# Kernel optimization log

Hardware: AMD Instinct MI355X
Metric: run time of the kernel (lower is better)

The kernel has to match this reference:

```python
import jax, jax.numpy as jnp
import numpy as np

EPS = 1e-16
LOG_2PI = float(np.log(2.0 * np.pi))
DUMMY = -2.0 * float(np.log(10.0))  # dummy component logit / log-prob


def setup_inputs() -> dict:
    key = jax.random.key(0)
    k1, k2, k3, k4, k5 = jax.random.split(key, 5)
    B, N, V, D = 32, 1024, 512, 4
    x = jax.random.normal(k1, (B, N, D), dtype=jnp.float32)
    votes = jax.random.normal(k2, (B, V, D), dtype=jnp.float32)
    # positive stds in [0.1, 1.0)
    scales = jax.random.uniform(k3, (B, V), dtype=jnp.float32) * 0.9 + 0.1
    vote_presence_prob = jax.random.uniform(k4, (B, V), dtype=jnp.float32)
    presence = jax.random.uniform(k5, (B, N), dtype=jnp.float32)
    return {"x": x, "votes": votes, "scales": scales,
            "vote_presence_prob": vote_presence_prob,
            "presence": presence, "n_votes": 16}


def reference(x, votes, scales, vote_presence_prob, presence, n_votes):
    B, N, D = x.shape
    V = votes.shape[1]
    # Broadcast Normal log-prob: x [B,N,1,D] vs votes [B,1,V,D], scale [B,1,V,1]
    sig = scales[:, None, :, None]
    z = (x[:, :, None, :] - votes[:, None, :, :]) / sig
    lp_per_dim = -0.5 * z * z - jnp.log(sig) - 0.5 * LOG_2PI
    vote_log_prob = jnp.sum(lp_per_dim, axis=-1)                       # [B,N,V]
    vote_log_prob = jnp.concatenate(
        [vote_log_prob, jnp.full((B, N, 1), DUMMY, vote_log_prob.dtype)], axis=2)  # [B,N,V+1]

    mixing_logits = jnp.log(vote_presence_prob + EPS)                  # safe_log, [B,V]
    mixing_logits = jnp.concatenate(
        [mixing_logits, jnp.full((B, 1), DUMMY, mixing_logits.dtype)], axis=1)     # [B,V+1]
    mixing_log_prob = jax.nn.log_softmax(mixing_logits, axis=1)        # [B,V+1]

    posterior = mixing_log_prob[:, None, :] + vote_log_prob            # [B,N,V+1]
    mixture_lp_per_comp = jax.scipy.special.logsumexp(posterior, axis=2)  # [B,N]
    mixture_lp_per_comp = mixture_lp_per_comp * presence
    log_prob = jnp.sum(mixture_lp_per_comp)                            # scalar

    winning_vote_idx = jnp.argmax(posterior[:, :, :-1], axis=2)        # [B,N]
    winner = jnp.take_along_axis(votes, winning_vote_idx[:, :, None], axis=1)  # [B,N,D]
    winner_pres = jnp.take_along_axis(vote_presence_prob, winning_vote_idx, axis=1)  # [B,N]
    vote_presence = (mixing_logits[:, :-1] > mixing_logits[:, -1:]).astype(jnp.float32)  # [B,V]
    is_from_capsule = winning_vote_idx // n_votes                      # [B,N]
    posterior_mixing_probs = jax.nn.softmax(posterior, axis=-1)[..., :-1]  # [B,N,V]

    return (log_prob, vote_presence, winner, winner_pres, is_from_capsule,
            mixing_logits, mixing_log_prob, jnp.zeros_like(winner),
            jnp.zeros_like(winner_pres), posterior_mixing_probs)
```

## Files before the change

kernel.cpp:

```cpp
#include <hip/hip_runtime.h>

typedef float v2f __attribute__((ext_vector_type(2)));

#define FEPS 1e-16f
#define LOG_2PI 1.8378770664093453f
#define DUMMYV -4.605170185988091f
#define LOG2E 1.4426950408889634f
#define LN2 0.6931471805599453f

constexpr int B = 32, N = 1024, V = 512;

constexpr long long OFF_LOGPROB    = 0;
constexpr long long OFF_VOTEPRES   = 1;
constexpr long long OFF_WINNER     = OFF_VOTEPRES + (long long)B * V;
constexpr long long OFF_WINNERPRES = OFF_WINNER + (long long)B * N * 4;
constexpr long long OFF_ISFROM     = OFF_WINNERPRES + (long long)B * N;
constexpr long long OFF_MLOGITS    = OFF_ISFROM + (long long)B * N;
constexpr long long OFF_MLOGPROB   = OFF_MLOGITS + (long long)B * (V + 1);
constexpr long long OFF_ZW         = OFF_MLOGPROB + (long long)B * (V + 1);
constexpr long long OFF_ZWP        = OFF_ZW + (long long)B * N * 4;
constexpr long long OFF_PMP        = OFF_ZWP + (long long)B * N;

__device__ __forceinline__ float fexp2(float x) {
#if __has_builtin(__builtin_amdgcn_exp2f)
    return __builtin_amdgcn_exp2f(x);
#else
    return __expf(x * LN2);
#endif
}
__device__ __forceinline__ float frcp(float x) {
#if __has_builtin(__builtin_amdgcn_rcpf)
    return __builtin_amdgcn_rcpf(x);
#else
    return 1.0f / x;
#endif
}

template<int RN> __device__ __forceinline__ float dppRorF(float x) {
    return __int_as_float(__builtin_amdgcn_update_dpp(
        0, __float_as_int(x), 0x120 | RN, 0xF, 0xF, false));
}
template<int RN> __device__ __forceinline__ int dppRorI(int x) {
    return __builtin_amdgcn_update_dpp(0, x, 0x120 | RN, 0xF, 0xF, false);
}

__device__ __forceinline__ float waveMaxF(float m) {
    m = fmaxf(m, dppRorF<1>(m));
    m = fmaxf(m, dppRorF<2>(m));
    m = fmaxf(m, dppRorF<4>(m));
    m = fmaxf(m, dppRorF<8>(m));
    m = fmaxf(m, __shfl_xor(m, 16));
    m = fmaxf(m, __shfl_xor(m, 32));
    return m;
}
__device__ __forceinline__ float waveSumF(float s) {
    s += dppRorF<1>(s);
    s += dppRorF<2>(s);
    s += dppRorF<4>(s);
    s += dppRorF<8>(s);
    s += __shfl_xor(s, 16);
    s += __shfl_xor(s, 32);
    return s;
}
__device__ __forceinline__ int waveMinI(int v) {
    int o;
    o = dppRorI<1>(v); v = o < v ? o : v;
    o = dppRorI<2>(v); v = o < v ? o : v;
    o = dppRorI<4>(v); v = o < v ? o : v;
    o = dppRorI<8>(v); v = o < v ? o : v;
    o = __shfl_xor(v, 16); v = o < v ? o : v;
    o = __shfl_xor(v, 32); v = o < v ? o : v;
    return v;
}

__global__ __launch_bounds__(256) void k_fused(const float* __restrict__ x,
                                               const float* __restrict__ votes,
                                               const float* __restrict__ scales,
                                               const float* __restrict__ vpp,
                                               const float* __restrict__ presence,
                                               const int* __restrict__ nvp,
                                               float* __restrict__ out,
                                               float* __restrict__ ws) {
    __shared__ float s_part[4];
    const int b = blockIdx.y, t = threadIdx.x, w = t >> 6, lane = t & 63;
    const long long bV = (long long)b * V;
    const float4* votes4 = reinterpret_cast<const float4*>(votes) + bV;

    float lg[8], lsv[8];
    float4 vt[8];
    #pragma unroll
    for (int k = 0; k < 8; ++k) {
        int v = k * 64 + lane;
        vt[k]  = votes4[v];
        lsv[k] = scales[bV + v];
        lg[k]  = __logf(vpp[bV + v] + FEPS);
    }

    float mm = lg[0];
    #pragma unroll
    for (int k = 1; k < 8; ++k) mm = fmaxf(mm, lg[k]);
    float M = fmaxf(waveMaxF(mm), DUMMYV);
    float ss = 0.f;
    #pragma unroll
    for (int k = 0; k < 8; ++k) ss += __expf(lg[k] - M);
    float S = waveSumF(ss) + __expf(DUMMYV - M);
    float lse = M + __logf(S);
    float dummy_post = DUMMYV + (DUMMYV - lse);

    if (blockIdx.x == 0 && w == 0) {
        #pragma unroll
        for (int k = 0; k < 8; ++k) {
            int v = k * 64 + lane;
            out[OFF_MLOGITS  + (long long)b * (V + 1) + v] = lg[k];
            out[OFF_MLOGPROB + (long long)b * (V + 1) + v] = lg[k] - lse;
            out[OFF_VOTEPRES + bV + v] = (lg[k] > DUMMYV) ? 1.0f : 0.0f;
        }
        if (lane == 0) {
            out[OFF_MLOGITS  + (long long)b * (V + 1) + V] = DUMMYV;
            out[OFF_MLOGPROB + (long long)b * (V + 1) + V] = DUMMYV - lse;
        }
    }

    v2f c2[4], hk[4], hvx[4], hvy[4], hvz[4], hvw[4];
    #pragma unroll
    for (int i = 0; i < 4; ++i) {
        float cc[2], kk[2], ax[2], ay[2], az[2], aw[2];
        #pragma unroll
        for (int h = 0; h < 2; ++h) {
            int k = 2 * i + h;
            float sv  = lsv[k];
            float inv = frcp(sv);
            float hh  = 0.5f * inv * inv;
            float c   = lg[k] - 4.0f * __logf(sv) - 2.0f * LOG_2PI - lse;
            float4 vv = vt[k];
            float v2  = vv.x * vv.x + vv.y * vv.y + vv.z * vv.z + vv.w * vv.w;
            cc[h] = (c - hh * v2 - dummy_post) * LOG2E;
            kk[h] = -hh * LOG2E;
            float g = 2.0f * hh * LOG2E;
            ax[h] = g * vv.x; ay[h] = g * vv.y; az[h] = g * vv.z; aw[h] = g * vv.w;
        }
        c2[i].x = cc[0];  c2[i].y = cc[1];
        hk[i].x = kk[0];  hk[i].y = kk[1];
        hvx[i].x = ax[0]; hvx[i].y = ax[1];
        hvy[i].x = ay[0]; hvy[i].y = ay[1];
        hvz[i].x = az[0]; hvz[i].y = az[1];
        hvw[i].x = aw[0]; hvw[i].y = aw[1];
    }

    const float4* x4 = reinterpret_cast<const float4*>(x) + (long long)b * N;
    const long long pmpB = OFF_PMP + ((long long)b * N) * V;
    int nv = nvp[0];
    float acc = 0.f;

    #pragma unroll 2
    for (int iter = 0; iter < 8; ++iter) {
        int n = blockIdx.x * 32 + iter * 4 + w;
        long long bn = (long long)b * N + n;
        float4 xv = x4[n];
        float px2 = xv.x * xv.x + xv.y * xv.y + xv.z * xv.z + xv.w * xv.w;
        v2f P2; P2.x = px2;  P2.y = px2;
        v2f Xx; Xx.x = xv.x; Xx.y = xv.x;
        v2f Xy; Xy.x = xv.y; Xy.y = xv.y;
        v2f Xz; Xz.x = xv.z; Xz.y = xv.z;
        v2f Xw; Xw.x = xv.w; Xw.y = xv.w;

        float p2s[8];
        #pragma unroll
        for (int i = 0; i < 4; ++i) {
            v2f tt = c2[i];
            tt += hk[i]  * P2;
            tt += hvx[i] * Xx;
            tt += hvy[i] * Xy;
            tt += hvz[i] * Xz;
            tt += hvw[i] * Xw;
            p2s[2 * i]     = tt.x;
            p2s[2 * i + 1] = tt.y;
        }

        float t1 = fmaxf(fmaxf(p2s[0], p2s[1]), p2s[2]);
        float t2 = fmaxf(fmaxf(p2s[3], p2s[4]), p2s[5]);
        float t3 = fmaxf(fmaxf(p2s[6], p2s[7]), t1);
        float m_in = fmaxf(t2, t3);
        float Mrow = waveMaxF(m_in);

        int kw = 7;
        #pragma unroll
        for (int k = 6; k >= 0; --k) kw = (p2s[k] == Mrow) ? k : kw;
        int cand = (m_in == Mrow) ? (kw * 64 + lane) : 0x7fffffff;
        int bi = waveMinI(cand);

        float e[8];
        float se = 0.f;
        #pragma unroll
        for (int k = 0; k < 8; ++k) { e[k] = fexp2(p2s[k]); se += e[k]; }
        se = waveSumF(se);
        float total = se + 1.0f;
        float rt = frcp(total);

        long long pb = pmpB + (long long)n * V;
        #pragma unroll
        for (int k = 0; k < 8; ++k)
            out[pb + k * 64 + lane] = e[k] * rt;

        if (lane == 0) {
            acc += (dummy_post + LN2 * __log2f(total)) * presence[bn];
            float4 wv = votes4[bi];
            out[OFF_WINNER + bn * 4 + 0] = wv.x;
            out[OFF_WINNER + bn * 4 + 1] = wv.y;
            out[OFF_WINNER + bn * 4 + 2] = wv.z;
            out[OFF_WINNER + bn * 4 + 3] = wv.w;
            out[OFF_WINNERPRES + bn]     = vpp[bV + bi];
            out[OFF_ISFROM + bn]         = (float)((nv == 16) ? (bi >> 4) : (bi / nv));
        }
        if (lane == 1) {
            out[OFF_ZW + bn * 4 + 0] = 0.f;
            out[OFF_ZW + bn * 4 + 1] = 0.f;
            out[OFF_ZW + bn * 4 + 2] = 0.f;
            out[OFF_ZW + bn * 4 + 3] = 0.f;
            out[OFF_ZWP + bn]        = 0.f;
        }
    }

    if (lane == 0) s_part[w] = acc;
    __syncthreads();
    if (t == 0)
        ws[(long long)b * gridDim.x + blockIdx.x] =
            s_part[0] + s_part[1] + s_part[2] + s_part[3];
}

__global__ __launch_bounds__(256) void k_reduce(const float* __restrict__ ws,
                                                float* __restrict__ out, int count) {
    __shared__ float sred[256];
    int t = threadIdx.x;
    float s = 0.f;
    for (int i = t; i < count; i += 256) s += ws[i];
    sred[t] = s;
    __syncthreads();
    for (int o = 128; o > 0; o >>= 1) {
        if (t < o) sred[t] += sred[t + o];
        __syncthreads();
    }
    if (t == 0) out[OFF_LOGPROB] = sred[0];
}

extern "C" void kernel_launch(void* const* d_in, const int* in_sizes, int n_in,
                              void* d_out, int out_size, void* d_ws, size_t ws_size,
                              hipStream_t stream) {
    const float* x        = (const float*)d_in[0];
    const float* votes    = (const float*)d_in[1];
    const float* scales   = (const float*)d_in[2];
    const float* vpp      = (const float*)d_in[3];
    const float* presence = (const float*)d_in[4];
    const int*   nv       = (const int*)d_in[5];
    float* out = (float*)d_out;
    float* ws  = (float*)d_ws;

    dim3 g(N / 32, B);
    k_fused<<<g, 256, 0, stream>>>(x, votes, scales, vpp, presence, nv, out, ws);
    k_reduce<<<1, 256, 0, stream>>>(ws, out, (N / 32) * B);
}
```

Before: 26.76 us.

## Remap vote-to-lane layout for 16-byte nontemporal stores and faster wave reductions

Each lane now owns four consecutive votes instead of four votes strided by 64. This lets the posterior-probability row be written with 16-byte nontemporal vector stores. The output base sits at an odd offset, so the layout is shifted by 3 floats to keep those stores 16-byte aligned, and lane 63 handles the wrapped tail with scalar and 2-wide stores. Wave reductions use ds_swizzle and permlane32_swap in place of the shfl steps, and the argmax tie-break now takes the minimum vote index directly. The cost is per-vote index bookkeeping and a divergent tail path on one lane.

```diff
diff --git a/kernel.cpp b/kernel.cpp
--- a/kernel.cpp
+++ b/kernel.cpp
@@ -1,6 +1,7 @@
 #include <hip/hip_runtime.h>
 
 typedef float v2f __attribute__((ext_vector_type(2)));
+typedef float v4f __attribute__((ext_vector_type(4)));
 
 #define FEPS 1e-16f
 #define LOG_2PI 1.8378770664093453f
@@ -43,24 +44,48 @@
 template<int RN> __device__ __forceinline__ int dppRorI(int x) {
     return __builtin_amdgcn_update_dpp(0, x, 0x120 | RN, 0xF, 0xF, false);
 }
+__device__ __forceinline__ float swz16F(float x) {
+    return __int_as_float(__builtin_amdgcn_ds_swizzle(__float_as_int(x), 0x401F));
+}
+__device__ __forceinline__ int swz16I(int x) {
+    return __builtin_amdgcn_ds_swizzle(x, 0x401F);
+}
+
+#if __has_builtin(__builtin_amdgcn_permlane32_swap)
+__device__ __forceinline__ float maxSwap32(float x) {
+    auto r = __builtin_amdgcn_permlane32_swap(__float_as_uint(x), __float_as_uint(x), false, false);
+    return fmaxf(__uint_as_float(r[0]), __uint_as_float(r[1]));
+}
+__device__ __forceinline__ float sumSwap32(float x) {
+    auto r = __builtin_amdgcn_permlane32_swap(__float_as_uint(x), __float_as_uint(x), false, false);
+    return __uint_as_float(r[0]) + __uint_as_float(r[1]);
+}
+__device__ __forceinline__ int minSwap32(int x) {
+    auto r = __builtin_amdgcn_permlane32_swap((unsigned)x, (unsigned)x, false, false);
+    int a = (int)r[0], b = (int)r[1];
+    return a < b ? a : b;
+}
+#else
+__device__ __forceinline__ float maxSwap32(float x) { return fmaxf(x, __shfl_xor(x, 32)); }
+__device__ __forceinline__ float sumSwap32(float x) { return x + __shfl_xor(x, 32); }
+__device__ __forceinline__ int   minSwap32(int x)   { int o = __shfl_xor(x, 32); return o < x ? o : x; }
+#endif
 
 __device__ __forceinline__ float waveMaxF(float m) {
     m = fmaxf(m, dppRorF<1>(m));
     m = fmaxf(m, dppRorF<2>(m));
     m = fmaxf(m, dppRorF<4>(m));
     m = fmaxf(m, dppRorF<8>(m));
-    m = fmaxf(m, __shfl_xor(m, 16));
-    m = fmaxf(m, __shfl_xor(m, 32));
-    return m;
+    m = fmaxf(m, swz16F(m));
+    return maxSwap32(m);
 }
 __device__ __forceinline__ float waveSumF(float s) {
     s += dppRorF<1>(s);
     s += dppRorF<2>(s);
     s += dppRorF<4>(s);
     s += dppRorF<8>(s);
-    s += __shfl_xor(s, 16);
-    s += __shfl_xor(s, 32);
-    return s;
+    s += swz16F(s);
+    return sumSwap32(s);
 }
 __device__ __forceinline__ int waveMinI(int v) {
     int o;
@@ -68,9 +93,8 @@
     o = dppRorI<2>(v); v = o < v ? o : v;
     o = dppRorI<4>(v); v = o < v ? o : v;
     o = dppRorI<8>(v); v = o < v ? o : v;
-    o = __shfl_xor(v, 16); v = o < v ? o : v;
-    o = __shfl_xor(v, 32); v = o < v ? o : v;
-    return v;
+    o = swz16I(v);     v = o < v ? o : v;
+    return minSwap32(v);
 }
 
 __global__ __launch_bounds__(256) void k_fused(const float* __restrict__ x,
@@ -86,11 +110,22 @@
     const long long bV = (long long)b * V;
     const float4* votes4 = reinterpret_cast<const float4*>(votes) + bV;
 
+    int vidx[8];
     float lg[8], lsv[8];
     float4 vt[8];
     #pragma unroll
-    for (int k = 0; k < 8; ++k) {
-        int v = k * 64 + lane;
+    for (int k = 0; k < 4; ++k) {
+        int v = 3 + 4 * lane + k;
+        vidx[k] = v;
+        vt[k]  = votes4[v];
+        lsv[k] = scales[bV + v];
+        lg[k]  = __logf(vpp[bV + v] + FEPS);
+    }
+    const int vtop[4] = {511, 0, 1, 2};
+    #pragma unroll
+    for (int k = 4; k < 8; ++k) {
+        int v = (lane < 63) ? (259 + 4 * lane + (k - 4)) : vtop[k - 4];
+        vidx[k] = v;
         vt[k]  = votes4[v];
         lsv[k] = scales[bV + v];
         lg[k]  = __logf(vpp[bV + v] + FEPS);
@@ -110,7 +145,7 @@
     if (blockIdx.x == 0 && w == 0) {
         #pragma unroll
         for (int k = 0; k < 8; ++k) {
-            int v = k * 64 + lane;
+            int v = vidx[k];
             out[OFF_MLOGITS  + (long long)b * (V + 1) + v] = lg[k];
             out[OFF_MLOGPROB + (long long)b * (V + 1) + v] = lg[k] - lse;
             out[OFF_VOTEPRES + bV + v] = (lg[k] > DUMMYV) ? 1.0f : 0.0f;
@@ -148,7 +183,6 @@
     }
 
     const float4* x4 = reinterpret_cast<const float4*>(x) + (long long)b * N;
-    const long long pmpB = OFF_PMP + ((long long)b * N) * V;
     int nv = nvp[0];
     float acc = 0.f;
 
@@ -180,13 +214,12 @@
         float t1 = fmaxf(fmaxf(p2s[0], p2s[1]), p2s[2]);
         float t2 = fmaxf(fmaxf(p2s[3], p2s[4]), p2s[5]);
         float t3 = fmaxf(fmaxf(p2s[6], p2s[7]), t1);
-        float m_in = fmaxf(t2, t3);
-        float Mrow = waveMaxF(m_in);
-
-        int kw = 7;
-        #pragma unroll
-        for (int k = 6; k >= 0; --k) kw = (p2s[k] == Mrow) ? k : kw;
-        int cand = (m_in == Mrow) ? (kw * 64 + lane) : 0x7fffffff;
+        float Mrow = waveMaxF(fmaxf(t2, t3));
+
+        int cand = 0x7fffffff;
+        #pragma unroll
+        for (int k = 0; k < 8; ++k)
+            if (p2s[k] == Mrow && vidx[k] < cand) cand = vidx[k];
         int bi = waveMinI(cand);
 
         float e[8];
@@ -197,10 +230,18 @@
         float total = se + 1.0f;
         float rt = frcp(total);
 
-        long long pb = pmpB + (long long)n * V;
-        #pragma unroll
-        for (int k = 0; k < 8; ++k)
-            out[pb + k * 64 + lane] = e[k] * rt;
+        float* rp = out + OFF_PMP + bn * (long long)V;
+        v4f qa; qa.x = e[0] * rt; qa.y = e[1] * rt; qa.z = e[2] * rt; qa.w = e[3] * rt;
+        v4f qb; qb.x = e[4] * rt; qb.y = e[5] * rt; qb.z = e[6] * rt; qb.w = e[7] * rt;
+        __builtin_nontemporal_store(qa, reinterpret_cast<v4f*>(rp + 3 + 4 * lane));
+        if (lane < 63) {
+            __builtin_nontemporal_store(qb, reinterpret_cast<v4f*>(rp + 259 + 4 * lane));
+        } else {
+            rp[511] = qb.x;
+            rp[0]   = qb.y;
+            v2f ez; ez.x = qb.z; ez.y = qb.w;
+            *reinterpret_cast<v2f*>(rp + 1) = ez;
+        }
 
         if (lane == 0) {
             acc += (dummy_post + LN2 * __log2f(total)) * presence[bn];
```

New measurement: 28.17 us. +5.3%, slower.
